# Kernel optimization log

Measured on AMD Instinct MI355X. Metric: run time of the kernel, lower is better.

Reference implementation:

```python
import jax, jax.numpy as jnp
import numpy as np

N, C, T, V, S, IC = 128, 256, 32, 25, 3, 64  # batch, channels, frames, joints, subsets, inter_channels
EPS = 1e-5


def conv1x1(x, w, b):
    # x: [N,C,T,V], w: [O,C], b: [O]
    return jnp.einsum('nctv,oc->notv', x, w) + b[None, :, None, None]


def bn(x, g, be, m, v):
    # eval-mode BatchNorm2d over channel dim
    inv = g / jnp.sqrt(v + EPS)
    return x * inv[None, :, None, None] + (be - m * inv)[None, :, None, None]


def pe_spatial(c, v):
    # spatial positional encoding: position = joint id, same for every frame
    div = jnp.exp(jnp.arange(0, c, 2).astype(jnp.float32) * (-(np.log(10000.0) / c)))
    ang = jnp.arange(v, dtype=jnp.float32)[:, None] * div[None, :]  # [V, C/2]
    pe = jnp.stack([jnp.sin(ang), jnp.cos(ang)], axis=-1).reshape(v, c)  # interleave sin/cos -> [V,C]
    return pe.T[None, :, None, :]  # [1,C,1,V]


def setup_inputs() -> dict:
    key = jax.random.key(0)
    ks = jax.random.split(key, 40)
    rn = lambda i, sh, s=1.0: jax.random.normal(ks[i], sh, dtype=jnp.float32) * s
    ru = lambda i, sh: jax.random.uniform(ks[i], sh, dtype=jnp.float32, minval=0.5, maxval=1.5)
    d = {
        'x': rn(0, (N, C, T, V)),
        'in_w': rn(1, (2 * S * IC, C), 0.05), 'in_b': rn(2, (2 * S * IC,), 0.05),
        'alphas': jnp.ones((1, S, 1, 1), jnp.float32),
        'attention0s': jnp.ones((1, S, V, V), jnp.float32) / V,
        'out_w': rn(3, (C, S * C), 0.02), 'out_b': rn(4, (C,), 0.02),
    }
    i = 5
    for p, (ci, co) in [('d1', (C, C)), ('d2', (C, C)), ('ff', (C, C))]:
        d[p + '_w'] = rn(i, (co, ci), 0.05); i += 1
        d[p + '_b'] = rn(i, (co,), 0.05); i += 1
    for p in ['out', 'd1', 'd2', 'ff']:
        d[p + '_g'] = 1.0 + rn(i, (C,), 0.1); i += 1
        d[p + '_be'] = rn(i, (C,), 0.1); i += 1
        d[p + '_m'] = rn(i, (C,), 0.1); i += 1
        d[p + '_v'] = ru(i, (C,)); i += 1
    return d


def reference(x, in_w, in_b, alphas, attention0s, out_w, out_b,
              d1_w, d1_b, d2_w, d2_b, ff_w, ff_b,
              out_g, out_be, out_m, out_v,
              d1_g, d1_be, d1_m, d1_v,
              d2_g, d2_be, d2_m, d2_v,
              ff_g, ff_be, ff_m, ff_v):
    n, c, t, v = x.shape
    lrelu = lambda z: jnp.where(z >= 0, z, 0.1 * z)
    # spatial positional encoding
    y = x + pe_spatial(c, v)
    # QK projection via 1x1 conv, split into q,k: [N,S,IC,T,V]
    qk = conv1x1(y, in_w, in_b).reshape(n, 2 * S, IC, t, v)
    q, k = qk[:, :S], qk[:, S:]
    # tanh-based attention score + learnable global attention (atts buffer is zeros)
    att = jnp.tanh(jnp.einsum('nsctu,nsctv->nsuv', q, k) / (IC * t)) * alphas
    att = att + attention0s  # broadcast over batch (dropout p=0 -> identity)
    # aggregate: [N,S,C,T,V] -> [N, S*C, T, V]
    y = jnp.einsum('nctu,nsuv->nsctv', x, att).reshape(n, S * c, t, v)
    # out_nets: conv1x1 + BN
    y = bn(conv1x1(y, out_w, out_b), out_g, out_be, out_m, out_v)
    # residual 1
    y = lrelu(bn(conv1x1(x, d1_w, d1_b), d1_g, d1_be, d1_m, d1_v) + y)
    # ff_nets: conv1x1 + BN + LeakyReLU
    y = lrelu(bn(conv1x1(y, ff_w, ff_b), ff_g, ff_be, ff_m, ff_v))
    # residual 2
    y = lrelu(bn(conv1x1(x, d2_w, d2_b), d2_g, d2_be, d2_m, d2_v) + y)
    return y
```

## Files before the change

kernel.cpp:

```cpp
#include <hip/hip_runtime.h>

typedef unsigned short u16;
typedef __bf16 bf16x8 __attribute__((ext_vector_type(8)));
typedef float f32x4 __attribute__((ext_vector_type(4)));

constexpr int NB = 128;
constexpr int CC = 256;
constexpr int TT = 32;
constexpr int VV = 25;
constexpr int SSS = 3;
constexpr int PIX = 800;
constexpr float EPSV = 1e-5f;

constexpr size_t OFF_PE  = 0;
constexpr size_t OFF_W1  = 64*1024;
constexpr size_t OFF_WK2 = OFF_W1  + 256*1024;
constexpr size_t OFF_WFF = OFF_WK2 + 512*1024;
constexpr size_t OFF_WD2 = OFF_WFF + 128*1024;
constexpr size_t OFF_B1  = OFF_WD2 + 128*1024;
constexpr size_t OFF_BK2 = OFF_B1  + 48*1024;
constexpr size_t OFF_BFF = OFF_BK2 + 4096;
constexpr size_t OFF_BD2 = OFF_BFF + 4096;
constexpr size_t OFF_ATT = 2ull*1024*1024;
constexpr size_t OFF_XB  = 4ull*1024*1024;
constexpr size_t OFF_BIG = OFF_XB + 52428800ull;
constexpr size_t OFF_Y3  = OFF_BIG + 157286400ull;

__device__ __forceinline__ float bf2f(u16 h) {
  union { unsigned u; float f; } c; c.u = ((unsigned)h) << 16; return c.f;
}
__device__ __forceinline__ u16 f2bf(float f) {
  union { float f; unsigned u; } c; c.f = f;
  unsigned r = c.u + 0x7fffu + ((c.u >> 16) & 1u);
  return (u16)(r >> 16);
}
__device__ __forceinline__ float lrelu(float z) { return z >= 0.f ? z : 0.1f*z; }

__global__ void prep_k(
    const float* __restrict__ in_w,  const float* __restrict__ in_b,
    const float* __restrict__ out_w, const float* __restrict__ out_b,
    const float* __restrict__ d1_w,  const float* __restrict__ d1_b,
    const float* __restrict__ d2_w,  const float* __restrict__ d2_b,
    const float* __restrict__ ff_w,  const float* __restrict__ ff_b,
    const float* __restrict__ out_g, const float* __restrict__ out_be, const float* __restrict__ out_m, const float* __restrict__ out_v,
    const float* __restrict__ d1_g,  const float* __restrict__ d1_be,  const float* __restrict__ d1_m,  const float* __restrict__ d1_v,
    const float* __restrict__ d2_g,  const float* __restrict__ d2_be,  const float* __restrict__ d2_m,  const float* __restrict__ d2_v,
    const float* __restrict__ ff_g,  const float* __restrict__ ff_be,  const float* __restrict__ ff_m,  const float* __restrict__ ff_v,
    float* __restrict__ pe, u16* __restrict__ w1b,
    u16* __restrict__ wk2, float* __restrict__ bk2,
    u16* __restrict__ wff, float* __restrict__ bff,
    u16* __restrict__ wd2, float* __restrict__ bd2,
    u16* __restrict__ qkb)
{
  const int id  = blockIdx.x*blockDim.x + threadIdx.x;
  const int nth = gridDim.x*blockDim.x;
  for (int i = id; i < CC*VV; i += nth) {
    int ch = i / VV, vv = i - ch*VV;
    int j = ch >> 1;
    float ang = (float)vv * expf((float)j * (-2.0f*logf(10000.0f)/(float)CC));
    pe[i] = (ch & 1) ? cosf(ang) : sinf(ang);
  }
  for (int i = id; i < 384*CC; i += nth) w1b[i] = f2bf(in_w[i]);
  for (int i = id; i < CC*1024; i += nth) {
    int o = i >> 10, k = i & 1023;
    float w;
    if (k < 768) { float inv = out_g[o]*rsqrtf(out_v[o]+EPSV); w = out_w[o*768+k]*inv; }
    else         { float inv = d1_g[o]*rsqrtf(d1_v[o]+EPSV);   w = d1_w[o*256+(k-768)]*inv; }
    wk2[i] = f2bf(w);
  }
  for (int i = id; i < CC*CC; i += nth) {
    int o = i >> 8;
    wff[i] = f2bf(ff_w[i]*(ff_g[o]*rsqrtf(ff_v[o]+EPSV)));
    wd2[i] = f2bf(d2_w[i]*(d2_g[o]*rsqrtf(d2_v[o]+EPSV)));
  }
  for (int i = id; i < CC; i += nth) {
    float invo = out_g[i]*rsqrtf(out_v[i]+EPSV);
    float invd = d1_g[i]*rsqrtf(d1_v[i]+EPSV);
    bk2[i] = out_b[i]*invo + out_be[i] - out_m[i]*invo
           + d1_b[i]*invd  + d1_be[i]  - d1_m[i]*invd;
    float invf = ff_g[i]*rsqrtf(ff_v[i]+EPSV);
    bff[i] = ff_b[i]*invf + ff_be[i] - ff_m[i]*invf;
    float inv2 = d2_g[i]*rsqrtf(d2_v[i]+EPSV);
    bd2[i] = d2_b[i]*inv2 + d2_be[i] - d2_m[i]*inv2;
  }
  for (int i = id; i < NB*TT*7*384; i += nth) {
    int ch = i % 384; int r = i / 384;
    int pr = r % 7; int t = (r/7) % TT; int n = r / (7*TT);
    qkb[((size_t)n*1024 + (size_t)t*32 + 25 + pr)*384 + ch] = 0;
  }
}

__global__ __launch_bounds__(256) void prep2_k(
    const float* __restrict__ in_w, const float* __restrict__ in_b,
    const float* __restrict__ pe, float* __restrict__ b1v)
{
  const int i = blockIdx.x*blockDim.x + threadIdx.x;
  if (i >= 384*VV) return;
  const int o = i % 384, v = i / 384;
  float acc = in_b[o];
  for (int c = 0; c < CC; ++c) acc += in_w[o*CC+c]*pe[c*VV+v];
  b1v[v*384+o] = acc;
}

__global__ __launch_bounds__(256) void k0_cvt(
    const float* __restrict__ x, u16* __restrict__ xb)
{
  __shared__ float xt[CC*VV];
  const int t = blockIdx.x, n = blockIdx.y;
  const float* xs = x + (size_t)n*CC*PIX + t*VV;
  for (int f = threadIdx.x; f < CC*VV; f += 256) {
    int c = f / VV, u = f - c*VV;
    xt[f] = xs[(size_t)c*PIX + u];
  }
  __syncthreads();
  const int c = threadIdx.x;
  u16* xrow = xb + ((size_t)n*PIX + t*VV)*CC + c;
  #pragma unroll
  for (int u = 0; u < VV; ++u)
    xrow[(size_t)u*CC] = f2bf(xt[c*VV+u]);
}

__global__ __launch_bounds__(64) void att_k(
    const u16* __restrict__ qkb, const float* __restrict__ alphas,
    const float* __restrict__ att0, u16* __restrict__ attb)
{
  const int s = blockIdx.x, n = blockIdx.y, lane = threadIdx.x;
  const u16* qb = qkb + (size_t)n*1024*384 + s*64;
  const u16* kb = qb + 192;
  f32x4 acc[2][2];
  #pragma unroll
  for (int i = 0; i < 2; ++i)
    #pragma unroll
    for (int j = 0; j < 2; ++j) acc[i][j] = f32x4{0.f,0.f,0.f,0.f};

  for (int t = 0; t < TT; ++t) {
    const u16* qrow = qb + (size_t)t*32*384;
    const u16* krow = kb + (size_t)t*32*384;
    #pragma unroll
    for (int ks = 0; ks < 2; ++ks) {
      const int ko = ks*32 + (lane>>4)*8;
      bf16x8 a0 = *(const bf16x8*)(qrow + (size_t)(lane&15)*384 + ko);
      bf16x8 a1 = *(const bf16x8*)(qrow + (size_t)(16+(lane&15))*384 + ko);
      bf16x8 b0 = *(const bf16x8*)(krow + (size_t)(lane&15)*384 + ko);
      bf16x8 b1 = *(const bf16x8*)(krow + (size_t)(16+(lane&15))*384 + ko);
      acc[0][0] = __builtin_amdgcn_mfma_f32_16x16x32_bf16(a0, b0, acc[0][0], 0,0,0);
      acc[0][1] = __builtin_amdgcn_mfma_f32_16x16x32_bf16(a0, b1, acc[0][1], 0,0,0);
      acc[1][0] = __builtin_amdgcn_mfma_f32_16x16x32_bf16(a1, b0, acc[1][0], 0,0,0);
      acc[1][1] = __builtin_amdgcn_mfma_f32_16x16x32_bf16(a1, b1, acc[1][1], 0,0,0);
    }
  }
  const float alpha = alphas[s];
  const float sc = 1.0f/2048.0f;
  u16* ab = attb + ((size_t)n*SSS + s)*1024;
  #pragma unroll
  for (int fm = 0; fm < 2; ++fm)
    #pragma unroll
    for (int fn = 0; fn < 2; ++fn)
      #pragma unroll
      for (int j = 0; j < 4; ++j) {
        int u = fm*16 + (lane>>4)*4 + j;
        int v = fn*16 + (lane&15);
        float val = 0.f;
        if (u < VV && v < VV)
          val = tanhf(acc[fm][fn][j]*sc)*alpha + att0[s*VV*VV + u*VV + v];
        ab[v*32 + u] = f2bf(val);
      }
}

__global__ __launch_bounds__(256) void p_k2(
    const u16* __restrict__ xb, const u16* __restrict__ attb, u16* __restrict__ Pb)
{
  __shared__ u16 Xs[CC*40];
  __shared__ u16 Al[SSS*32*40];
  const int t = blockIdx.x, n = blockIdx.y;
  const u16* xrow = xb + ((size_t)n*PIX + t*VV)*CC;
  for (int f = threadIdx.x; f < VV*CC; f += 256) {
    int u = f >> 8, c = f & 255;
    Xs[c*40+u] = xrow[(size_t)u*CC + c];
  }
  for (int idx = threadIdx.x; idx < CC*7; idx += 256) {
    int c = idx / 7, u = 25 + idx % 7;
    Xs[c*40+u] = 0;
  }
  const u16* ab = attb + (size_t)n*SSS*1024;
  for (int f = threadIdx.x; f < SSS*1024; f += 256) {
    int sv = f >> 5, u = f & 31;
    Al[sv*40+u] = ab[f];
  }
  __syncthreads();

  const int lane = threadIdx.x & 63, w = threadIdx.x >> 6;
  const int cb0 = w*64;
  const int k0 = (lane>>4)*8;
  const int r15 = lane & 15;
  f32x4 acc[SSS][4][2];
  #pragma unroll
  for (int s = 0; s < SSS; ++s)
    #pragma unroll
    for (int mt = 0; mt < 4; ++mt)
      #pragma unroll
      for (int nt = 0; nt < 2; ++nt) acc[s][mt][nt] = f32x4{0.f,0.f,0.f,0.f};

  #pragma unroll
  for (int s = 0; s < SSS; ++s) {
    bf16x8 b0 = *(const bf16x8*)&Al[((s*32) + r15)*40 + k0];
    bf16x8 b1 = *(const bf16x8*)&Al[((s*32) + 16 + r15)*40 + k0];
    #pragma unroll
    for (int mt = 0; mt < 4; ++mt) {
      bf16x8 a = *(const bf16x8*)&Xs[(cb0 + mt*16 + r15)*40 + k0];
      acc[s][mt][0] = __builtin_amdgcn_mfma_f32_16x16x32_bf16(a, b0, acc[s][mt][0], 0,0,0);
      acc[s][mt][1] = __builtin_amdgcn_mfma_f32_16x16x32_bf16(a, b1, acc[s][mt][1], 0,0,0);
    }
  }

  const int j4 = (lane>>4)*4;
  #pragma unroll
  for (int s = 0; s < SSS; ++s)
    #pragma unroll
    for (int nt = 0; nt < 2; ++nt) {
      const int v = nt*16 + r15;
      if (v < VV) {
        u16* dst0 = Pb + ((size_t)n*PIX + t*VV + v)*768 + s*CC + cb0 + j4;
        #pragma unroll
        for (int mt = 0; mt < 4; ++mt) {
          f32x4 a = acc[s][mt][nt];
          ushort4 st; st.x=f2bf(a[0]); st.y=f2bf(a[1]); st.z=f2bf(a[2]); st.w=f2bf(a[3]);
          *(ushort4*)(dst0 + mt*16) = st;
        }
      }
    }
}

template<int KTOT, int NKC0, int BS0, int BS1, int EPI>
__global__ __launch_bounds__(512, 1)
void gemm_k(const u16* __restrict__ W, const float* __restrict__ bias,
            const u16* __restrict__ B0, const u16* __restrict__ B1,
            void* __restrict__ outv, const u16* __restrict__ y4b)
{
  constexpr int NKC = KTOT/64;
  __shared__ u16 As[2][128*64];
  __shared__ u16 Bs[2][160*64];
  const int tid = threadIdx.x;
  const int lane = tid & 63, wid = tid >> 6;
  const int wm = wid >> 1, wn = wid & 1;
  const int pt = blockIdx.x, mt = blockIdx.y, n = blockIdx.z;
  const int m0 = mt*128, p0 = pt*160;
  const int lr = lane >> 3;
  const int lc = (((lane & 7) ^ lr)) * 8;

  f32x4 acc[2][5];
  #pragma unroll
  for (int i = 0; i < 2; ++i)
    #pragma unroll
    for (int j = 0; j < 5; ++j) acc[i][j] = f32x4{0.f,0.f,0.f,0.f};

  auto stage = [&](int buf, int kc) {
    const u16* wsrc = W + (size_t)m0*KTOT + (size_t)kc*64;
    for (int g = wid; g < 16; g += 8) {
      const u16* src = wsrc + (size_t)(g*8 + lr)*KTOT + lc;
      __builtin_amdgcn_global_load_lds(
          (const __attribute__((address_space(1))) void*)src,
          (__attribute__((address_space(3))) void*)(&As[buf][g*512]), 16, 0, 0);
    }
    const u16* bbase; int bs;
    if (NKC0 >= NKC || kc < NKC0) {
      bbase = B0 + ((size_t)n*PIX + p0)*BS0 + (size_t)kc*64; bs = BS0;
    } else {
      bbase = B1 + ((size_t)n*PIX + p0)*BS1 + (size_t)(kc-NKC0)*64; bs = BS1;
    }
    for (int g = wid; g < 20; g += 8) {
      const u16* src = bbase + (size_t)(g*8 + lr)*bs + lc;
      __builtin_amdgcn_global_load_lds(
          (const __attribute__((address_space(1))) void*)src,
          (__attribute__((address_space(3))) void*)(&Bs[buf][g*512]), 16, 0, 0);
    }
  };

  auto compute = [&](int buf) {
    const int par = lane & 7;
    const int gq  = lane >> 4;
    const int r15 = lane & 15;
    #pragma unroll
    for (int ks = 0; ks < 2; ++ks) {
      const int ko = (((ks*4 + gq) ^ par)) * 8;
      bf16x8 a0 = *(const bf16x8*)&As[buf][(wm*32 + r15)*64 + ko];
      bf16x8 a1 = *(const bf16x8*)&As[buf][(wm*32 + 16 + r15)*64 + ko];
      bf16x8 bfr[5];
      #pragma unroll
      for (int fn = 0; fn < 5; ++fn)
        bfr[fn] = *(const bf16x8*)&Bs[buf][(wn*80 + fn*16 + r15)*64 + ko];
      #pragma unroll
      for (int fn = 0; fn < 5; ++fn) {
        acc[0][fn] = __builtin_amdgcn_mfma_f32_16x16x32_bf16(a0, bfr[fn], acc[0][fn], 0,0,0);
        acc[1][fn] = __builtin_amdgcn_mfma_f32_16x16x32_bf16(a1, bfr[fn], acc[1][fn], 0,0,0);
      }
    }
  };

  stage(0, 0);
  __syncthreads();
  for (int kc = 0; kc < NKC; ++kc) {
    if (kc + 1 < NKC) stage((kc+1)&1, kc+1);
    compute(kc&1);
    __syncthreads();
  }

  const int oc = (lane>>4)*4, pc = lane&15;
  #pragma unroll
  for (int fm = 0; fm < 2; ++fm) {
    const int o = m0 + wm*32 + fm*16 + oc;
    #pragma unroll
    for (int fn = 0; fn < 5; ++fn) {
      const int p = p0 + wn*80 + fn*16 + pc;
      f32x4 v = acc[fm][fn];
      float4 bv;
      if constexpr (EPI == 0) bv = *(const float4*)&bias[(p % VV)*384 + o];
      else                    bv = *(const float4*)&bias[o];
      float r0 = v[0]+bv.x, r1 = v[1]+bv.y, r2 = v[2]+bv.z, r3 = v[3]+bv.w;
      if constexpr (EPI == 0) {
        int row = (p/VV)*32 + (p%VV);
        ushort4 st; st.x=f2bf(r0); st.y=f2bf(r1); st.z=f2bf(r2); st.w=f2bf(r3);
        *(ushort4*)((u16*)outv + ((size_t)n*1024 + row)*384 + o) = st;
      } else if constexpr (EPI == 1) {
        ushort4 st;
        st.x=f2bf(lrelu(r0)); st.y=f2bf(lrelu(r1)); st.z=f2bf(lrelu(r2)); st.w=f2bf(lrelu(r3));
        *(ushort4*)((u16*)outv + ((size_t)n*PIX + p)*256 + o) = st;
      } else if constexpr (EPI == 2) {
        u16* op = (u16*)outv + ((size_t)n*256 + o)*PIX + p;
        op[0]      = f2bf(lrelu(r0));
        op[PIX]    = f2bf(lrelu(r1));
        op[2*PIX]  = f2bf(lrelu(r2));
        op[3*PIX]  = f2bf(lrelu(r3));
      } else {
        const u16* yp = y4b + ((size_t)n*256 + o)*PIX + p;
        float* op = (float*)outv + ((size_t)n*256 + o)*PIX + p;
        op[0]      = lrelu(r0 + bf2f(yp[0]));
        op[PIX]    = lrelu(r1 + bf2f(yp[PIX]));
        op[2*PIX]  = lrelu(r2 + bf2f(yp[2*PIX]));
        op[3*PIX]  = lrelu(r3 + bf2f(yp[3*PIX]));
      }
    }
  }
}

extern "C" void kernel_launch(void* const* d_in, const int* in_sizes, int n_in,
                              void* d_out, int out_size, void* d_ws, size_t ws_size,
                              hipStream_t stream)
{
  const float* x      = (const float*)d_in[0];
  const float* in_w   = (const float*)d_in[1];
  const float* in_b   = (const float*)d_in[2];
  const float* alphas = (const float*)d_in[3];
  const float* att0   = (const float*)d_in[4];
  const float* out_w  = (const float*)d_in[5];
  const float* out_b  = (const float*)d_in[6];
  const float* d1_w   = (const float*)d_in[7];
  const float* d1_b   = (const float*)d_in[8];
  const float* d2_w   = (const float*)d_in[9];
  const float* d2_b   = (const float*)d_in[10];
  const float* ff_w   = (const float*)d_in[11];
  const float* ff_b   = (const float*)d_in[12];
  const float* out_g  = (const float*)d_in[13];
  const float* out_be = (const float*)d_in[14];
  const float* out_m  = (const float*)d_in[15];
  const float* out_v  = (const float*)d_in[16];
  const float* d1_g   = (const float*)d_in[17];
  const float* d1_be  = (const float*)d_in[18];
  const float* d1_m   = (const float*)d_in[19];
  const float* d1_v   = (const float*)d_in[20];
  const float* d2_g   = (const float*)d_in[21];
  const float* d2_be  = (const float*)d_in[22];
  const float* d2_m   = (const float*)d_in[23];
  const float* d2_v   = (const float*)d_in[24];
  const float* ff_g   = (const float*)d_in[25];
  const float* ff_be  = (const float*)d_in[26];
  const float* ff_m   = (const float*)d_in[27];
  const float* ff_v   = (const float*)d_in[28];

  char* ws = (char*)d_ws;
  float* pe  = (float*)(ws + OFF_PE);
  u16*  w1b  = (u16*)(ws + OFF_W1);
  u16*  wk2  = (u16*)(ws + OFF_WK2);
  u16*  wff  = (u16*)(ws + OFF_WFF);
  u16*  wd2  = (u16*)(ws + OFF_WD2);
  float* b1v = (float*)(ws + OFF_B1);
  float* bk2 = (float*)(ws + OFF_BK2);
  float* bff = (float*)(ws + OFF_BFF);
  float* bd2 = (float*)(ws + OFF_BD2);
  u16*  attb = (u16*)(ws + OFF_ATT);
  u16*  xb   = (u16*)(ws + OFF_XB);
  u16*  qkb  = (u16*)(ws + OFF_BIG);
  u16*  Pb   = (u16*)(ws + OFF_BIG);
  u16*  y4b  = (u16*)(ws + OFF_BIG);
  u16*  y3b  = (u16*)(ws + OFF_Y3);

  prep_k<<<256, 256, 0, stream>>>(
      in_w, in_b, out_w, out_b, d1_w, d1_b, d2_w, d2_b, ff_w, ff_b,
      out_g, out_be, out_m, out_v, d1_g, d1_be, d1_m, d1_v,
      d2_g, d2_be, d2_m, d2_v, ff_g, ff_be, ff_m, ff_v,
      pe, w1b, wk2, bk2, wff, bff, wd2, bd2, qkb);

  prep2_k<<<(384*VV + 255)/256, 256, 0, stream>>>(in_w, in_b, pe, b1v);

  k0_cvt<<<dim3(TT, NB), 256, 0, stream>>>(x, xb);

  gemm_k<256, 4, 256, 256, 0><<<dim3(5, 3, NB), 512, 0, stream>>>(w1b, b1v, xb, xb, qkb, nullptr);

  att_k<<<dim3(SSS, NB), 64, 0, stream>>>(qkb, alphas, att0, attb);

  p_k2<<<dim3(TT, NB), 256, 0, stream>>>(xb, attb, Pb);

  gemm_k<1024, 12, 768, 256, 1><<<dim3(5, 2, NB), 512, 0, stream>>>(wk2, bk2, Pb, xb, y3b, nullptr);

  gemm_k<256, 4, 256, 256, 2><<<dim3(5, 2, NB), 512, 0, stream>>>(wff, bff, y3b, y3b, y4b, nullptr);

  gemm_k<256, 4, 256, 256, 3><<<dim3(5, 2, NB), 512, 0, stream>>>(wd2, bd2, xb, xb, d_out, y4b);
}
```

Measured before the change: 613.6 us.

## Fuse ff and d2 GEMMs into one kernel and split attention reduction over warps

The final ff GEMM and d2 residual GEMM now run in one kernel that keeps two accumulator sets over the same output tile. It streams the d2 weight/x K-chunks, then the ff weight/y3 chunks, and applies both epilogues together. This removes the bf16 y4 intermediate round trip and one kernel launch, at the cost of twice the accumulator registers. The attention-score kernel also now uses four waves, each summing over a quarter of the frames, with the partial sums combined through shared memory for more parallelism.

```diff
diff --git a/kernel.cpp b/kernel.cpp
--- a/kernel.cpp
+++ b/kernel.cpp
@@ -120,11 +120,13 @@
     xrow[(size_t)u*CC] = f2bf(xt[c*VV+u]);
 }
 
-__global__ __launch_bounds__(64) void att_k(
+__global__ __launch_bounds__(256) void att_k(
     const u16* __restrict__ qkb, const float* __restrict__ alphas,
     const float* __restrict__ att0, u16* __restrict__ attb)
 {
-  const int s = blockIdx.x, n = blockIdx.y, lane = threadIdx.x;
+  __shared__ float red[3][64][17];
+  const int s = blockIdx.x, n = blockIdx.y;
+  const int lane = threadIdx.x & 63, w = threadIdx.x >> 6;
   const u16* qb = qkb + (size_t)n*1024*384 + s*64;
   const u16* kb = qb + 192;
   f32x4 acc[2][2];
@@ -133,7 +135,7 @@
     #pragma unroll
     for (int j = 0; j < 2; ++j) acc[i][j] = f32x4{0.f,0.f,0.f,0.f};
 
-  for (int t = 0; t < TT; ++t) {
+  for (int t = w; t < TT; t += 4) {
     const u16* qrow = qb + (size_t)t*32*384;
     const u16* krow = kb + (size_t)t*32*384;
     #pragma unroll
@@ -149,22 +151,46 @@
       acc[1][1] = __builtin_amdgcn_mfma_f32_16x16x32_bf16(a1, b1, acc[1][1], 0,0,0);
     }
   }
-  const float alpha = alphas[s];
-  const float sc = 1.0f/2048.0f;
-  u16* ab = attb + ((size_t)n*SSS + s)*1024;
-  #pragma unroll
-  for (int fm = 0; fm < 2; ++fm)
-    #pragma unroll
-    for (int fn = 0; fn < 2; ++fn)
-      #pragma unroll
-      for (int j = 0; j < 4; ++j) {
-        int u = fm*16 + (lane>>4)*4 + j;
-        int v = fn*16 + (lane&15);
-        float val = 0.f;
-        if (u < VV && v < VV)
-          val = tanhf(acc[fm][fn][j]*sc)*alpha + att0[s*VV*VV + u*VV + v];
-        ab[v*32 + u] = f2bf(val);
-      }
+  if (w > 0) {
+    float* dst = &red[w-1][lane][0];
+    #pragma unroll
+    for (int fm = 0; fm < 2; ++fm)
+      #pragma unroll
+      for (int fn = 0; fn < 2; ++fn)
+        #pragma unroll
+        for (int j = 0; j < 4; ++j)
+          dst[(fm*2+fn)*4+j] = acc[fm][fn][j];
+  }
+  __syncthreads();
+  if (w == 0) {
+    #pragma unroll
+    for (int r = 0; r < 3; ++r) {
+      const float* src = &red[r][lane][0];
+      #pragma unroll
+      for (int fm = 0; fm < 2; ++fm)
+        #pragma unroll
+        for (int fn = 0; fn < 2; ++fn)
+          #pragma unroll
+          for (int j = 0; j < 4; ++j)
+            acc[fm][fn][j] += src[(fm*2+fn)*4+j];
+    }
+    const float alpha = alphas[s];
+    const float sc = 1.0f/2048.0f;
+    u16* ab = attb + ((size_t)n*SSS + s)*1024;
+    #pragma unroll
+    for (int fm = 0; fm < 2; ++fm)
+      #pragma unroll
+      for (int fn = 0; fn < 2; ++fn)
+        #pragma unroll
+        for (int j = 0; j < 4; ++j) {
+          int u = fm*16 + (lane>>4)*4 + j;
+          int v = fn*16 + (lane&15);
+          float val = 0.f;
+          if (u < VV && v < VV)
+            val = tanhf(acc[fm][fn][j]*sc)*alpha + att0[s*VV*VV + u*VV + v];
+          ab[v*32 + u] = f2bf(val);
+        }
+  }
 }
 
 __global__ __launch_bounds__(256) void p_k2(
@@ -235,7 +261,7 @@
 __global__ __launch_bounds__(512, 1)
 void gemm_k(const u16* __restrict__ W, const float* __restrict__ bias,
             const u16* __restrict__ B0, const u16* __restrict__ B1,
-            void* __restrict__ outv, const u16* __restrict__ y4b)
+            void* __restrict__ outv)
 {
   constexpr int NKC = KTOT/64;
   __shared__ u16 As[2][128*64];
@@ -321,24 +347,103 @@
         int row = (p/VV)*32 + (p%VV);
         ushort4 st; st.x=f2bf(r0); st.y=f2bf(r1); st.z=f2bf(r2); st.w=f2bf(r3);
         *(ushort4*)((u16*)outv + ((size_t)n*1024 + row)*384 + o) = st;
-      } else if constexpr (EPI == 1) {
+      } else {
         ushort4 st;
         st.x=f2bf(lrelu(r0)); st.y=f2bf(lrelu(r1)); st.z=f2bf(lrelu(r2)); st.w=f2bf(lrelu(r3));
         *(ushort4*)((u16*)outv + ((size_t)n*PIX + p)*256 + o) = st;
-      } else if constexpr (EPI == 2) {
-        u16* op = (u16*)outv + ((size_t)n*256 + o)*PIX + p;
-        op[0]      = f2bf(lrelu(r0));
-        op[PIX]    = f2bf(lrelu(r1));
-        op[2*PIX]  = f2bf(lrelu(r2));
-        op[3*PIX]  = f2bf(lrelu(r3));
-      } else {
-        const u16* yp = y4b + ((size_t)n*256 + o)*PIX + p;
-        float* op = (float*)outv + ((size_t)n*256 + o)*PIX + p;
-        op[0]      = lrelu(r0 + bf2f(yp[0]));
-        op[PIX]    = lrelu(r1 + bf2f(yp[PIX]));
-        op[2*PIX]  = lrelu(r2 + bf2f(yp[2*PIX]));
-        op[3*PIX]  = lrelu(r3 + bf2f(yp[3*PIX]));
       }
+    }
+  }
+}
+
+__global__ __launch_bounds__(512, 1)
+void gemm2_k(const u16* __restrict__ WD2, const u16* __restrict__ WFF,
+             const float* __restrict__ bd2, const float* __restrict__ bff,
+             const u16* __restrict__ XB, const u16* __restrict__ Y3B,
+             float* __restrict__ outp)
+{
+  __shared__ u16 As[2][128*64];
+  __shared__ u16 Bs[2][160*64];
+  const int tid = threadIdx.x;
+  const int lane = tid & 63, wid = tid >> 6;
+  const int wm = wid >> 1, wn = wid & 1;
+  const int pt = blockIdx.x, mt = blockIdx.y, n = blockIdx.z;
+  const int m0 = mt*128, p0 = pt*160;
+  const int lr = lane >> 3;
+  const int lc = (((lane & 7) ^ lr)) * 8;
+
+  f32x4 accD[2][5], accF[2][5];
+  #pragma unroll
+  for (int i = 0; i < 2; ++i)
+    #pragma unroll
+    for (int j = 0; j < 5; ++j) { accD[i][j] = f32x4{0.f,0.f,0.f,0.f}; accF[i][j] = f32x4{0.f,0.f,0.f,0.f}; }
+
+  auto stage = [&](int buf, int kc) {
+    const int kk = kc & 3;
+    const u16* Wb = (kc < 4) ? WD2 : WFF;
+    const u16* Bb = (kc < 4) ? XB  : Y3B;
+    const u16* wsrc = Wb + (size_t)m0*256 + (size_t)kk*64;
+    for (int g = wid; g < 16; g += 8) {
+      const u16* src = wsrc + (size_t)(g*8 + lr)*256 + lc;
+      __builtin_amdgcn_global_load_lds(
+          (const __attribute__((address_space(1))) void*)src,
+          (__attribute__((address_space(3))) void*)(&As[buf][g*512]), 16, 0, 0);
+    }
+    const u16* bbase = Bb + ((size_t)n*PIX + p0)*256 + (size_t)kk*64;
+    for (int g = wid; g < 20; g += 8) {
+      const u16* src = bbase + (size_t)(g*8 + lr)*256 + lc;
+      __builtin_amdgcn_global_load_lds(
+          (const __attribute__((address_space(1))) void*)src,
+          (__attribute__((address_space(3))) void*)(&Bs[buf][g*512]), 16, 0, 0);
+    }
+  };
+
+  auto compute = [&](int buf, f32x4 (&acc)[2][5]) {
+    const int par = lane & 7;
+    const int gq  = lane >> 4;
+    const int r15 = lane & 15;
+    #pragma unroll
+    for (int ks = 0; ks < 2; ++ks) {
+      const int ko = (((ks*4 + gq) ^ par)) * 8;
+      bf16x8 a0 = *(const bf16x8*)&As[buf][(wm*32 + r15)*64 + ko];
+      bf16x8 a1 = *(const bf16x8*)&As[buf][(wm*32 + 16 + r15)*64 + ko];
+      bf16x8 bfr[5];
+      #pragma unroll
+      for (int fn = 0; fn < 5; ++fn)
+        bfr[fn] = *(const bf16x8*)&Bs[buf][(wn*80 + fn*16 + r15)*64 + ko];
+      #pragma unroll
+      for (int fn = 0; fn < 5; ++fn) {
+        acc[0][fn] = __builtin_amdgcn_mfma_f32_16x16x32_bf16(a0, bfr[fn], acc[0][fn], 0,0,0);
+        acc[1][fn] = __builtin_amdgcn_mfma_f32_16x16x32_bf16(a1, bfr[fn], acc[1][fn], 0,0,0);
+      }
+    }
+  };
+
+  stage(0, 0);
+  __syncthreads();
+  for (int kc = 0; kc < 8; ++kc) {
+    if (kc + 1 < 8) stage((kc+1)&1, kc+1);
+    if (kc < 4) compute(kc&1, accD); else compute(kc&1, accF);
+    __syncthreads();
+  }
+
+  const int oc = (lane>>4)*4, pc = lane&15;
+  #pragma unroll
+  for (int fm = 0; fm < 2; ++fm) {
+    const int o = m0 + wm*32 + fm*16 + oc;
+    const float4 bD = *(const float4*)&bd2[o];
+    const float4 bF = *(const float4*)&bff[o];
+    #pragma unroll
+    for (int fn = 0; fn < 5; ++fn) {
+      const int p = p0 + wn*80 + fn*16 + pc;
+      f32x4 vD = accD[fm][fn], vF = accF[fm][fn];
+      float y40 = lrelu(vF[0]+bF.x), y41 = lrelu(vF[1]+bF.y);
+      float y42 = lrelu(vF[2]+bF.z), y43 = lrelu(vF[3]+bF.w);
+      float* op = outp + ((size_t)n*256 + o)*PIX + p;
+      op[0]      = lrelu(vD[0] + bD.x + y40);
+      op[PIX]    = lrelu(vD[1] + bD.y + y41);
+      op[2*PIX]  = lrelu(vD[2] + bD.z + y42);
+      op[3*PIX]  = lrelu(vD[3] + bD.w + y43);
     }
   }
 }
@@ -391,7 +496,6 @@
   u16*  xb   = (u16*)(ws + OFF_XB);
   u16*  qkb  = (u16*)(ws + OFF_BIG);
   u16*  Pb   = (u16*)(ws + OFF_BIG);
-  u16*  y4b  = (u16*)(ws + OFF_BIG);
   u16*  y3b  = (u16*)(ws + OFF_Y3);
 
   prep_k<<<256, 256, 0, stream>>>(
@@ -404,15 +508,13 @@
 
   k0_cvt<<<dim3(TT, NB), 256, 0, stream>>>(x, xb);
 
-  gemm_k<256, 4, 256, 256, 0><<<dim3(5, 3, NB), 512, 0, stream>>>(w1b, b1v, xb, xb, qkb, nullptr);
-
-  att_k<<<dim3(SSS, NB), 64, 0, stream>>>(qkb, alphas, att0, attb);
+  gemm_k<256, 4, 256, 256, 0><<<dim3(5, 3, NB), 512, 0, stream>>>(w1b, b1v, xb, xb, qkb);
+
+  att_k<<<dim3(SSS, NB), 256, 0, stream>>>(qkb, alphas, att0, attb);
 
   p_k2<<<dim3(TT, NB), 256, 0, stream>>>(xb, attb, Pb);
 
-  gemm_k<1024, 12, 768, 256, 1><<<dim3(5, 2, NB), 512, 0, stream>>>(wk2, bk2, Pb, xb, y3b, nullptr);
-
-  gemm_k<256, 4, 256, 256, 2><<<dim3(5, 2, NB), 512, 0, stream>>>(wff, bff, y3b, y3b, y4b, nullptr);
-
-  gemm_k<256, 4, 256, 256, 3><<<dim3(5, 2, NB), 512, 0, stream>>>(wd2, bd2, xb, xb, d_out, y4b);
-}
+  gemm_k<1024, 12, 768, 256, 1><<<dim3(5, 2, NB), 512, 0, stream>>>(wk2, bk2, Pb, xb, y3b);
+
+  gemm2_k<<<dim3(5, 2, NB), 512, 0, stream>>>(wd2, wff, bd2, bff, xb, y3b, (float*)d_out);
+}
```

Measured after the change: 576.6 us. 1.06x faster.
